# Performance work log

Hardware: AMD Instinct MI355X
Metric: run time of the kernel (lower is better)

Reference implementation:

```python
import jax, jax.numpy as jnp
import numpy as np

B, S, DM, H, D = 2, 2048, 1024, 16, 64

def setup_inputs() -> dict:
    key = jax.random.key(0)
    ks = jax.random.split(key, 9)
    def g(k, shape, scale=0.02):
        return jax.random.normal(k, shape, dtype=jnp.float32) * scale
    return {
        "x":  jax.random.normal(ks[0], (B, S, DM), dtype=jnp.float32),
        "Wq": g(ks[1], (DM, H * D)), "bq": g(ks[2], (H * D,)),
        "Wk": g(ks[3], (DM, H * D)), "bk": g(ks[4], (H * D,)),
        "Wv": g(ks[5], (DM, H * D)), "bv": g(ks[6], (H * D,)),
        "Wo": g(ks[7], (H * D, DM)), "bo": g(ks[8], (DM,)),
    }

def reference(x, Wq, bq, Wk, bk, Wv, bv, Wo, bo):
    b, s, _ = x.shape
    # projections -> (B, H, S, D)
    q = (x @ Wq + bq).reshape(b, s, H, D).transpose(0, 2, 1, 3)
    k = (x @ Wk + bk).reshape(b, s, H, D).transpose(0, 2, 1, 3)
    v = (x @ Wv + bv).reshape(b, s, H, D).transpose(0, 2, 1, 3)
    # naive attention: full (B,H,S,S) scores, causal mask, softmax
    scores = jnp.einsum("bhqd,bhkd->bhqk", q, k) / jnp.sqrt(jnp.float32(D))
    causal = jnp.tril(jnp.ones((s, s), dtype=bool))
    scores = jnp.where(causal[None, None], scores, jnp.float32(-jnp.inf))
    weights = jax.nn.softmax(scores, axis=-1)
    out = jnp.einsum("bhqk,bhkd->bhqd", weights, v)  # (B,H,S,D)
    out = out.transpose(0, 2, 1, 3).reshape(b, s, H * D)
    return out @ Wo + bo  # dropout_p = 0 -> identity
```

## Files before the change

### kernel.cpp

```cpp
#include <hip/hip_runtime.h>
#include <hip/hip_bf16.h>

typedef __hip_bfloat16 bf16;
typedef __attribute__((ext_vector_type(8))) short bf16x8;
typedef __attribute__((ext_vector_type(4))) float f32x4;
typedef __attribute__((ext_vector_type(4))) unsigned int u32x4;

#define MFMA_BF16(a, b, c) __builtin_amdgcn_mfma_f32_16x16x32_bf16((a), (b), (c), 0, 0, 0)

static constexpr int B_  = 2;
static constexpr int S_  = 2048;
static constexpr int DM_ = 1024;
static constexpr int H_  = 16;
static constexpr int D_  = 64;
static constexpr int M_  = B_ * S_;

__device__ __forceinline__ void load16(const void* g, void* l) {
  __builtin_amdgcn_global_load_lds(
      (const __attribute__((address_space(1))) void*)g,
      (__attribute__((address_space(3))) void*)l, 16, 0, 0);
}

__device__ __forceinline__ unsigned int pack_bf16(float lo, float hi) {
  const unsigned int ul = __builtin_bit_cast(unsigned short, __float2bfloat16(lo));
  const unsigned int uh = __builtin_bit_cast(unsigned short, __float2bfloat16(hi));
  return (uh << 16) | ul;
}


__global__ void cvt_f32_bf16_kernel(const float* __restrict__ in,
                                    bf16* __restrict__ out, int n4) {
  int i = blockIdx.x * blockDim.x + threadIdx.x;
  if (i >= n4) return;
  float4 v = ((const float4*)in)[i];
  ushort4 u;
  u.x = __builtin_bit_cast(unsigned short, __float2bfloat16(v.x));
  u.y = __builtin_bit_cast(unsigned short, __float2bfloat16(v.y));
  u.z = __builtin_bit_cast(unsigned short, __float2bfloat16(v.z));
  u.w = __builtin_bit_cast(unsigned short, __float2bfloat16(v.w));
  ((ushort4*)out)[i] = u;
}

__global__ void transpose_cvt_kernel(const float* __restrict__ w0,
                                     const float* __restrict__ w1,
                                     const float* __restrict__ w2,
                                     const float* __restrict__ w3,
                                     bf16* __restrict__ o0, bf16* __restrict__ o1,
                                     bf16* __restrict__ o2, bf16* __restrict__ o3) {
  __shared__ float t[32][33];
  const float* in = blockIdx.z == 0 ? w0 : blockIdx.z == 1 ? w1 : blockIdx.z == 2 ? w2 : w3;
  bf16* out = blockIdx.z == 0 ? o0 : blockIdx.z == 1 ? o1 : blockIdx.z == 2 ? o2 : o3;
  int tx = threadIdx.x & 31;
  int ty = threadIdx.x >> 5;
  int r0 = blockIdx.y * 32;
  int c0 = blockIdx.x * 32;
#pragma unroll
  for (int yy = 0; yy < 32; yy += 8)
    t[ty + yy][tx] = in[(size_t)(r0 + ty + yy) * DM_ + c0 + tx];
  __syncthreads();
#pragma unroll
  for (int yy = 0; yy < 32; yy += 8)
    out[(size_t)(c0 + ty + yy) * DM_ + r0 + tx] = __float2bfloat16(t[tx][ty + yy]);
}

template <int MODE>
__global__ __launch_bounds__(256) void gemm_bt_kernel(
    const bf16* __restrict__ A, const bf16* __restrict__ Bt,
    const float* __restrict__ bias, const float* __restrict__ bias2,
    const float* __restrict__ bias3, void* __restrict__ out, int K) {
  __shared__ bf16 As[128 * 32];
  __shared__ bf16 Bs[128 * 32];
  const int tid = threadIdx.x;
  const int wid = tid >> 6, lane = tid & 63;
  const int g = lane >> 4, c = lane & 15;
  const int wr = wid >> 1, wc = wid & 1;
  const int bm = blockIdx.x, bn = blockIdx.y;

  f32x4 acc[4][4] = {};

  const char* Ag = (const char*)(A + (size_t)bm * 128 * K);
  const char* Bg = (const char*)(Bt + (size_t)bn * 128 * K);
  const int f0 = tid * 16, f1 = f0 + 4096;
  const int r0 = f0 >> 6, cb0 = f0 & 63;
  const int r1 = f1 >> 6;
  const size_t rowbytes = (size_t)K * 2;

  for (int kt = 0; kt < K / 32; ++kt) {
    const size_t koff = (size_t)kt * 64;
    load16(Ag + (size_t)r0 * rowbytes + koff + cb0, (char*)As + f0);
    load16(Ag + (size_t)r1 * rowbytes + koff + cb0, (char*)As + f1);
    load16(Bg + (size_t)r0 * rowbytes + koff + cb0, (char*)Bs + f0);
    load16(Bg + (size_t)r1 * rowbytes + koff + cb0, (char*)Bs + f1);
    __syncthreads();
    bf16x8 af[4], bfr[4];
#pragma unroll
    for (int mi = 0; mi < 4; ++mi)
      af[mi] = *(const bf16x8*)&As[(wr * 64 + mi * 16 + c) * 32 + g * 8];
#pragma unroll
    for (int ni = 0; ni < 4; ++ni)
      bfr[ni] = *(const bf16x8*)&Bs[(wc * 64 + ni * 16 + c) * 32 + g * 8];
#pragma unroll
    for (int mi = 0; mi < 4; ++mi)
#pragma unroll
      for (int ni = 0; ni < 4; ++ni)
        acc[mi][ni] = MFMA_BF16(af[mi], bfr[ni], acc[mi][ni]);
    __syncthreads();
  }

#pragma unroll
  for (int ni = 0; ni < 4; ++ni) {
    const int n_g = bn * 128 + wc * 64 + ni * 16 + c;
    float bv;
    if constexpr (MODE == 3) {
      const int proj = n_g >> 10, ncol = n_g & 1023;
      bv = proj == 0 ? bias[ncol] : proj == 1 ? bias2[ncol] : bias3[ncol];
    } else {
      bv = bias[n_g];
    }
#pragma unroll
    for (int mi = 0; mi < 4; ++mi) {
#pragma unroll
      for (int r = 0; r < 4; ++r) {
        const int m_g = bm * 128 + wr * 64 + mi * 16 + g * 4 + r;
        const float val = acc[mi][ni][r] + bv;
        if constexpr (MODE == 2) {
          ((float*)out)[(size_t)m_g * DM_ + n_g] = val;
        } else {
          const int proj = n_g >> 10, ncol = n_g & 1023;
          const int b = m_g >> 11, s = m_g & (S_ - 1);
          const int h = ncol >> 6, d = ncol & (D_ - 1);
          size_t idx = (size_t)proj * 4194304;
          if (proj < 2)
            idx += (((size_t)(b * H_ + h)) * S_ + s) * D_ + d;
          else
            idx += (((size_t)(b * H_ + h)) * D_ + d) * S_ + s;
          ((bf16*)out)[idx] = __float2bfloat16(val);
        }
      }
    }
  }
}

__global__ __launch_bounds__(256, 4) void flash_attn_kernel(
    const bf16* __restrict__ Q, const bf16* __restrict__ Kg,
    const bf16* __restrict__ Vt, bf16* __restrict__ Aout) {
  __shared__ bf16 Ks[2][64 * 64];
  __shared__ bf16 Vs[2][64 * 64];
  const int tid = threadIdx.x;
  const int w = tid >> 6, lane = tid & 63;
  const int g = lane >> 4, c = lane & 15;

  const int bid = blockIdx.x;
  const int xcd = bid & 7, loc = bid >> 3;
  const int bh = xcd * 4 + (loc & 3);
  const int j = 31 - (loc >> 2);
  const int t = j * 4 + w;
  const int b = bh >> 4, h = bh & (H_ - 1);

  const float ALPHA2 = 0.125f * 1.44269504f;
  const float THR2 = 11.5f;
  const float NEG_INF = -__builtin_inff();

  const char* Kbase = (const char*)(Kg + (size_t)bh * S_ * D_);
  const char* Vbase = (const char*)(Vt + (size_t)bh * D_ * S_);
  const int s0 = tid, s1 = tid + 256;
  const int sr0 = s0 >> 3, sq0 = ((s0 & 7) ^ (sr0 & 7)) << 4;
  const int sr1 = s1 >> 3, sq1 = ((s1 & 7) ^ (sr1 & 7)) << 4;

  const bf16* Qp = Q + ((size_t)bh * S_ + t * 16 + c) * D_;
  bf16x8 qf[2];
  qf[0] = *(const bf16x8*)&Qp[g * 8];
  qf[1] = *(const bf16x8*)&Qp[32 + g * 8];

  f32x4 o[4] = {};
  float m = -1000.0f;
  float lsum = 0.0f;

  const int rowlim = w * 16 + c;
  const int src0 = ((g & 1) * 2) * 16 + c;
  const int src1 = src0 + 16;
  const bool ghi = (g >= 2);
  const int cs = c & 7;
  int roff[2][4];
#pragma unroll
  for (int kk = 0; kk < 2; ++kk)
#pragma unroll
    for (int n = 0; n < 4; ++n)
      roff[kk][n] = n * 2048 + c * 128 + (((kk * 4 + g) ^ cs) << 4);

  {
    const char* Krow = Kbase;
    const char* Vcol = Vbase;
    load16(Krow + sr0 * 128 + sq0, (char*)Ks[0] + s0 * 16);
    load16(Krow + sr1 * 128 + sq1, (char*)Ks[0] + s1 * 16);
    load16(Vcol + sr0 * 4096 + sq0, (char*)Vs[0] + s0 * 16);
    load16(Vcol + sr1 * 4096 + sq1, (char*)Vs[0] + s1 * 16);
  }
  __syncthreads();

  int cur = 0;
#pragma unroll 1
  for (int kv = 0; kv <= j; ++kv) {
    if (kv < j) {
      const char* Krow = Kbase + (size_t)(kv + 1) * 8192;
      const char* Vcol = Vbase + (size_t)(kv + 1) * 128;
      const int nb = cur ^ 1;
      load16(Krow + sr0 * 128 + sq0, (char*)Ks[nb] + s0 * 16);
      load16(Krow + sr1 * 128 + sq1, (char*)Ks[nb] + s1 * 16);
      load16(Vcol + sr0 * 4096 + sq0, (char*)Vs[nb] + s0 * 16);
      load16(Vcol + sr1 * 4096 + sq1, (char*)Vs[nb] + s1 * 16);
    }

    const char* Kt = (const char*)Ks[cur];
    const char* Vtile = (const char*)Vs[cur];
    bf16x8 kf[2][4];
#pragma unroll
    for (int kk = 0; kk < 2; ++kk)
#pragma unroll
      for (int n = 0; n < 4; ++n)
        kf[kk][n] = *(const bf16x8*)(Kt + roff[kk][n]);

    f32x4 st[4] = {};
#pragma unroll
    for (int n = 0; n < 4; ++n) {
      st[n] = MFMA_BF16(kf[0][n], qf[0], st[n]);
      st[n] = MFMA_BF16(kf[1][n], qf[1], st[n]);
    }

    bf16x8 vf[2][4];
#pragma unroll
    for (int kk = 0; kk < 2; ++kk)
#pragma unroll
      for (int n = 0; n < 4; ++n)
        vf[kk][n] = *(const bf16x8*)(Vtile + roff[kk][n]);

    float a[4][4];
#pragma unroll
    for (int n = 0; n < 4; ++n)
#pragma unroll
      for (int r = 0; r < 4; ++r)
        a[n][r] = fmaf(st[n][r], ALPHA2, -m);
    if (kv == j) {
#pragma unroll
      for (int n = 0; n < 4; ++n)
#pragma unroll
        for (int r = 0; r < 4; ++r)
          if (n * 16 + g * 4 + r > rowlim) a[n][r] = NEG_INF;
    }

    float dm;
    {
      float t0 = fmaxf(fmaxf(a[0][0], a[0][1]), fmaxf(a[0][2], a[0][3]));
      float t1 = fmaxf(fmaxf(a[1][0], a[1][1]), fmaxf(a[1][2], a[1][3]));
      float t2 = fmaxf(fmaxf(a[2][0], a[2][1]), fmaxf(a[2][2], a[2][3]));
      float t3 = fmaxf(fmaxf(a[3][0], a[3][1]), fmaxf(a[3][2], a[3][3]));
      dm = fmaxf(fmaxf(t0, t1), fmaxf(t2, t3));
    }
    dm = fmaxf(dm, __shfl_xor(dm, 16, 64));
    dm = fmaxf(dm, __shfl_xor(dm, 32, 64));

    if (__any(dm > THR2)) {
      const float sh = fmaxf(dm, 0.0f);
      const float sc = __builtin_amdgcn_exp2f(-sh);
      m += sh;
      lsum *= sc;
#pragma unroll
      for (int n = 0; n < 4; ++n)
#pragma unroll
        for (int r = 0; r < 4; ++r) o[n][r] *= sc;
#pragma unroll
      for (int n = 0; n < 4; ++n)
#pragma unroll
        for (int r = 0; r < 4; ++r) a[n][r] -= sh;
    }

    float p[4][4];
#pragma unroll
    for (int n = 0; n < 4; ++n)
#pragma unroll
      for (int r = 0; r < 4; ++r) p[n][r] = __builtin_amdgcn_exp2f(a[n][r]);
    {
      float q0 = (p[0][0] + p[0][1]) + (p[0][2] + p[0][3]);
      float q1 = (p[1][0] + p[1][1]) + (p[1][2] + p[1][3]);
      float q2 = (p[2][0] + p[2][1]) + (p[2][2] + p[2][3]);
      float q3 = (p[3][0] + p[3][1]) + (p[3][2] + p[3][3]);
      lsum += (q0 + q1) + (q2 + q3);
    }

    unsigned int dw[4][2];
#pragma unroll
    for (int n = 0; n < 4; ++n) {
      dw[n][0] = pack_bf16(p[n][0], p[n][1]);
      dw[n][1] = pack_bf16(p[n][2], p[n][3]);
    }

#pragma unroll
    for (int kk = 0; kk < 2; ++kk) {
      unsigned int bb[4];
      {
        unsigned int lo = __shfl(dw[kk * 2][0], src0, 64);
        unsigned int hi = __shfl(dw[kk * 2 + 1][0], src0, 64);
        bb[0] = ghi ? hi : lo;
      }
      {
        unsigned int lo = __shfl(dw[kk * 2][1], src0, 64);
        unsigned int hi = __shfl(dw[kk * 2 + 1][1], src0, 64);
        bb[1] = ghi ? hi : lo;
      }
      {
        unsigned int lo = __shfl(dw[kk * 2][0], src1, 64);
        unsigned int hi = __shfl(dw[kk * 2 + 1][0], src1, 64);
        bb[2] = ghi ? hi : lo;
      }
      {
        unsigned int lo = __shfl(dw[kk * 2][1], src1, 64);
        unsigned int hi = __shfl(dw[kk * 2 + 1][1], src1, 64);
        bb[3] = ghi ? hi : lo;
      }
      u32x4 bbv = {bb[0], bb[1], bb[2], bb[3]};
      bf16x8 pb = __builtin_bit_cast(bf16x8, bbv);
#pragma unroll
      for (int n = 0; n < 4; ++n) o[n] = MFMA_BF16(vf[kk][n], pb, o[n]);
    }

    __syncthreads();
    cur ^= 1;
  }

  lsum += __shfl_xor(lsum, 16, 64);
  lsum += __shfl_xor(lsum, 32, 64);
  const float inv = 1.0f / lsum;

  bf16* Arow = Aout + ((size_t)b * S_ + t * 16 + c) * (H_ * D_) + h * D_;
#pragma unroll
  for (int n = 0; n < 4; ++n) {
    ushort4 u;
    u.x = __builtin_bit_cast(unsigned short, __float2bfloat16(o[n][0] * inv));
    u.y = __builtin_bit_cast(unsigned short, __float2bfloat16(o[n][1] * inv));
    u.z = __builtin_bit_cast(unsigned short, __float2bfloat16(o[n][2] * inv));
    u.w = __builtin_bit_cast(unsigned short, __float2bfloat16(o[n][3] * inv));
    *(ushort4*)&Arow[n * 16 + g * 4] = u;
  }
}


extern "C" void kernel_launch(void* const* d_in, const int* in_sizes, int n_in,
                              void* d_out, int out_size, void* d_ws, size_t ws_size,
                              hipStream_t stream) {
  (void)in_sizes; (void)n_in; (void)out_size; (void)ws_size;
  const float* x  = (const float*)d_in[0];
  const float* Wq = (const float*)d_in[1];
  const float* bq = (const float*)d_in[2];
  const float* Wk = (const float*)d_in[3];
  const float* bk = (const float*)d_in[4];
  const float* Wv = (const float*)d_in[5];
  const float* bv = (const float*)d_in[6];
  const float* Wo = (const float*)d_in[7];
  const float* bo = (const float*)d_in[8];
  float* out = (float*)d_out;

  char* ws = (char*)d_ws;
  bf16* xb  = (bf16*)(ws);
  bf16* Wqt = (bf16*)(ws + (8u << 20));
  bf16* Wkt = (bf16*)(ws + (10u << 20));
  bf16* Wvt = (bf16*)(ws + (12u << 20));
  bf16* Wot = (bf16*)(ws + (14u << 20));
  bf16* Qb  = (bf16*)(ws + (16u << 20));
  bf16* Kb  = (bf16*)(ws + (24u << 20));
  bf16* Vtb = (bf16*)(ws + (32u << 20));
  bf16* Ab  = xb;

  cvt_f32_bf16_kernel<<<4096, 256, 0, stream>>>(x, xb, (M_ * DM_) / 4);
  transpose_cvt_kernel<<<dim3(32, 32, 4), 256, 0, stream>>>(
      Wq, Wk, Wv, Wo, Wqt, Wkt, Wvt, Wot);

  gemm_bt_kernel<3><<<dim3(32, 24), 256, 0, stream>>>(
      xb, Wqt, bq, bk, bv, (void*)Qb, DM_);

  flash_attn_kernel<<<dim3(1024), 256, 0, stream>>>(Qb, Kb, Vtb, Ab);

  gemm_bt_kernel<2><<<dim3(32, 8), 256, 0, stream>>>(
      Ab, Wot, bo, nullptr, nullptr, (void*)out, DM_);
}
```

Before: 127.8 us.

## Pair causal query tiles per block and triple-buffer KV with setprio

Each attention block now handles two query tiles, j and 31-j, so causal work is balanced across blocks, and the grid is halved to 512. KV staging moves from a double to a triple buffer with a prefetch distance of two, explicit vmcnt waits and a single barrier per iteration. s_setprio is raised around the MFMA groups. The aim is to remove tail imbalance and hide load latency, at the cost of more LDS per block (48KB), which may limit occupancy, and half as many blocks.

```diff
diff --git a/kernel.cpp b/kernel.cpp
--- a/kernel.cpp
+++ b/kernel.cpp
@@ -144,8 +144,7 @@
 __global__ __launch_bounds__(256, 4) void flash_attn_kernel(
     const bf16* __restrict__ Q, const bf16* __restrict__ Kg,
     const bf16* __restrict__ Vt, bf16* __restrict__ Aout) {
-  __shared__ bf16 Ks[2][64 * 64];
-  __shared__ bf16 Vs[2][64 * 64];
+  __shared__ bf16 KVs[3][2][64 * 64];
   const int tid = threadIdx.x;
   const int w = tid >> 6, lane = tid & 63;
   const int g = lane >> 4, c = lane & 15;
@@ -153,8 +152,7 @@
   const int bid = blockIdx.x;
   const int xcd = bid & 7, loc = bid >> 3;
   const int bh = xcd * 4 + (loc & 3);
-  const int j = 31 - (loc >> 2);
-  const int t = j * 4 + w;
+  const int pp = loc >> 2;
   const int b = bh >> 4, h = bh & (H_ - 1);
 
   const float ALPHA2 = 0.125f * 1.44269504f;
@@ -167,14 +165,14 @@
   const int sr0 = s0 >> 3, sq0 = ((s0 & 7) ^ (sr0 & 7)) << 4;
   const int sr1 = s1 >> 3, sq1 = ((s1 & 7) ^ (sr1 & 7)) << 4;
 
-  const bf16* Qp = Q + ((size_t)bh * S_ + t * 16 + c) * D_;
-  bf16x8 qf[2];
-  qf[0] = *(const bf16x8*)&Qp[g * 8];
-  qf[1] = *(const bf16x8*)&Qp[32 + g * 8];
-
-  f32x4 o[4] = {};
-  float m = -1000.0f;
-  float lsum = 0.0f;
+  auto stageKV = [&](int kv, int bufi) {
+    const char* Krow = Kbase + (size_t)kv * 8192;
+    const char* Vcol = Vbase + (size_t)kv * 128;
+    load16(Krow + sr0 * 128 + sq0, (char*)KVs[bufi][0] + s0 * 16);
+    load16(Krow + sr1 * 128 + sq1, (char*)KVs[bufi][0] + s1 * 16);
+    load16(Vcol + sr0 * 4096 + sq0, (char*)KVs[bufi][1] + s0 * 16);
+    load16(Vcol + sr1 * 4096 + sq1, (char*)KVs[bufi][1] + s1 * 16);
+  };
 
   const int rowlim = w * 16 + c;
   const int src0 = ((g & 1) * 2) * 16 + c;
@@ -188,158 +186,169 @@
     for (int n = 0; n < 4; ++n)
       roff[kk][n] = n * 2048 + c * 128 + (((kk * 4 + g) ^ cs) << 4);
 
-  {
-    const char* Krow = Kbase;
-    const char* Vcol = Vbase;
-    load16(Krow + sr0 * 128 + sq0, (char*)Ks[0] + s0 * 16);
-    load16(Krow + sr1 * 128 + sq1, (char*)Ks[0] + s1 * 16);
-    load16(Vcol + sr0 * 4096 + sq0, (char*)Vs[0] + s0 * 16);
-    load16(Vcol + sr1 * 4096 + sq1, (char*)Vs[0] + s1 * 16);
-  }
-  __syncthreads();
-
-  int cur = 0;
 #pragma unroll 1
-  for (int kv = 0; kv <= j; ++kv) {
-    if (kv < j) {
-      const char* Krow = Kbase + (size_t)(kv + 1) * 8192;
-      const char* Vcol = Vbase + (size_t)(kv + 1) * 128;
-      const int nb = cur ^ 1;
-      load16(Krow + sr0 * 128 + sq0, (char*)Ks[nb] + s0 * 16);
-      load16(Krow + sr1 * 128 + sq1, (char*)Ks[nb] + s1 * 16);
-      load16(Vcol + sr0 * 4096 + sq0, (char*)Vs[nb] + s0 * 16);
-      load16(Vcol + sr1 * 4096 + sq1, (char*)Vs[nb] + s1 * 16);
+  for (int pass = 0; pass < 2; ++pass) {
+    const int j = pass == 0 ? pp : 31 - pp;
+    const int t16 = j * 4 + w;
+
+    const bf16* Qp = Q + ((size_t)bh * S_ + t16 * 16 + c) * D_;
+    bf16x8 qf[2];
+    qf[0] = *(const bf16x8*)&Qp[g * 8];
+    qf[1] = *(const bf16x8*)&Qp[32 + g * 8];
+
+    f32x4 o[4] = {};
+    float m = -1000.0f;
+    float lsum = 0.0f;
+
+    stageKV(0, 0);
+    if (j >= 1) stageKV(1, 1);
+
+    int cb = 0;
+#pragma unroll 1
+    for (int kv = 0; kv <= j; ++kv) {
+      if (kv < j) asm volatile("s_waitcnt vmcnt(4)" ::: "memory");
+      else        asm volatile("s_waitcnt vmcnt(0)" ::: "memory");
+      __builtin_amdgcn_s_barrier();
+      if (kv + 2 <= j) {
+        int sb = cb + 2; if (sb >= 3) sb -= 3;
+        stageKV(kv + 2, sb);
+      }
+
+      const char* Kt = (const char*)KVs[cb][0];
+      const char* Vtile = (const char*)KVs[cb][1];
+      bf16x8 kf[2][4];
+#pragma unroll
+      for (int kk = 0; kk < 2; ++kk)
+#pragma unroll
+        for (int n = 0; n < 4; ++n)
+          kf[kk][n] = *(const bf16x8*)(Kt + roff[kk][n]);
+
+      f32x4 st[4] = {};
+      __builtin_amdgcn_s_setprio(1);
+#pragma unroll
+      for (int n = 0; n < 4; ++n) {
+        st[n] = MFMA_BF16(kf[0][n], qf[0], st[n]);
+        st[n] = MFMA_BF16(kf[1][n], qf[1], st[n]);
+      }
+      __builtin_amdgcn_s_setprio(0);
+
+      bf16x8 vf[2][4];
+#pragma unroll
+      for (int kk = 0; kk < 2; ++kk)
+#pragma unroll
+        for (int n = 0; n < 4; ++n)
+          vf[kk][n] = *(const bf16x8*)(Vtile + roff[kk][n]);
+
+      float a[4][4];
+#pragma unroll
+      for (int n = 0; n < 4; ++n)
+#pragma unroll
+        for (int r = 0; r < 4; ++r)
+          a[n][r] = fmaf(st[n][r], ALPHA2, -m);
+      if (kv == j) {
+#pragma unroll
+        for (int n = 0; n < 4; ++n)
+#pragma unroll
+          for (int r = 0; r < 4; ++r)
+            if (n * 16 + g * 4 + r > rowlim) a[n][r] = NEG_INF;
+      }
+
+      float dm;
+      {
+        float t0 = fmaxf(fmaxf(a[0][0], a[0][1]), fmaxf(a[0][2], a[0][3]));
+        float t1 = fmaxf(fmaxf(a[1][0], a[1][1]), fmaxf(a[1][2], a[1][3]));
+        float t2 = fmaxf(fmaxf(a[2][0], a[2][1]), fmaxf(a[2][2], a[2][3]));
+        float t3 = fmaxf(fmaxf(a[3][0], a[3][1]), fmaxf(a[3][2], a[3][3]));
+        dm = fmaxf(fmaxf(t0, t1), fmaxf(t2, t3));
+      }
+      dm = fmaxf(dm, __shfl_xor(dm, 16, 64));
+      dm = fmaxf(dm, __shfl_xor(dm, 32, 64));
+
+      if (__any(dm > THR2)) {
+        const float sh = fmaxf(dm, 0.0f);
+        const float sc = __builtin_amdgcn_exp2f(-sh);
+        m += sh;
+        lsum *= sc;
+#pragma unroll
+        for (int n = 0; n < 4; ++n)
+#pragma unroll
+          for (int r = 0; r < 4; ++r) o[n][r] *= sc;
+#pragma unroll
+        for (int n = 0; n < 4; ++n)
+#pragma unroll
+          for (int r = 0; r < 4; ++r) a[n][r] -= sh;
+      }
+
+      float p[4][4];
+#pragma unroll
+      for (int n = 0; n < 4; ++n)
+#pragma unroll
+        for (int r = 0; r < 4; ++r) p[n][r] = __builtin_amdgcn_exp2f(a[n][r]);
+      {
+        float q0 = (p[0][0] + p[0][1]) + (p[0][2] + p[0][3]);
+        float q1 = (p[1][0] + p[1][1]) + (p[1][2] + p[1][3]);
+        float q2 = (p[2][0] + p[2][1]) + (p[2][2] + p[2][3]);
+        float q3 = (p[3][0] + p[3][1]) + (p[3][2] + p[3][3]);
+        lsum += (q0 + q1) + (q2 + q3);
+      }
+
+      unsigned int dw[4][2];
+#pragma unroll
+      for (int n = 0; n < 4; ++n) {
+        dw[n][0] = pack_bf16(p[n][0], p[n][1]);
+        dw[n][1] = pack_bf16(p[n][2], p[n][3]);
+      }
+
+#pragma unroll
+      for (int kk = 0; kk < 2; ++kk) {
+        unsigned int bb[4];
+        {
+          unsigned int lo = __shfl(dw[kk * 2][0], src0, 64);
+          unsigned int hi = __shfl(dw[kk * 2 + 1][0], src0, 64);
+          bb[0] = ghi ? hi : lo;
+        }
+        {
+          unsigned int lo = __shfl(dw[kk * 2][1], src0, 64);
+          unsigned int hi = __shfl(dw[kk * 2 + 1][1], src0, 64);
+          bb[1] = ghi ? hi : lo;
+        }
+        {
+          unsigned int lo = __shfl(dw[kk * 2][0], src1, 64);
+          unsigned int hi = __shfl(dw[kk * 2 + 1][0], src1, 64);
+          bb[2] = ghi ? hi : lo;
+        }
+        {
+          unsigned int lo = __shfl(dw[kk * 2][1], src1, 64);
+          unsigned int hi = __shfl(dw[kk * 2 + 1][1], src1, 64);
+          bb[3] = ghi ? hi : lo;
+        }
+        u32x4 bbv = {bb[0], bb[1], bb[2], bb[3]};
+        bf16x8 pb = __builtin_bit_cast(bf16x8, bbv);
+        __builtin_amdgcn_s_setprio(1);
+#pragma unroll
+        for (int n = 0; n < 4; ++n) o[n] = MFMA_BF16(vf[kk][n], pb, o[n]);
+        __builtin_amdgcn_s_setprio(0);
+      }
+
+      cb = (cb == 2) ? 0 : cb + 1;
     }
 
-    const char* Kt = (const char*)Ks[cur];
-    const char* Vtile = (const char*)Vs[cur];
-    bf16x8 kf[2][4];
-#pragma unroll
-    for (int kk = 0; kk < 2; ++kk)
-#pragma unroll
-      for (int n = 0; n < 4; ++n)
-        kf[kk][n] = *(const bf16x8*)(Kt + roff[kk][n]);
-
-    f32x4 st[4] = {};
+    lsum += __shfl_xor(lsum, 16, 64);
+    lsum += __shfl_xor(lsum, 32, 64);
+    const float inv = 1.0f / lsum;
+
+    bf16* Arow = Aout + ((size_t)b * S_ + t16 * 16 + c) * (H_ * D_) + h * D_;
 #pragma unroll
     for (int n = 0; n < 4; ++n) {
-      st[n] = MFMA_BF16(kf[0][n], qf[0], st[n]);
-      st[n] = MFMA_BF16(kf[1][n], qf[1], st[n]);
+      ushort4 u;
+      u.x = __builtin_bit_cast(unsigned short, __float2bfloat16(o[n][0] * inv));
+      u.y = __builtin_bit_cast(unsigned short, __float2bfloat16(o[n][1] * inv));
+      u.z = __builtin_bit_cast(unsigned short, __float2bfloat16(o[n][2] * inv));
+      u.w = __builtin_bit_cast(unsigned short, __float2bfloat16(o[n][3] * inv));
+      *(ushort4*)&Arow[n * 16 + g * 4] = u;
     }
 
-    bf16x8 vf[2][4];
-#pragma unroll
-    for (int kk = 0; kk < 2; ++kk)
-#pragma unroll
-      for (int n = 0; n < 4; ++n)
-        vf[kk][n] = *(const bf16x8*)(Vtile + roff[kk][n]);
-
-    float a[4][4];
-#pragma unroll
-    for (int n = 0; n < 4; ++n)
-#pragma unroll
-      for (int r = 0; r < 4; ++r)
-        a[n][r] = fmaf(st[n][r], ALPHA2, -m);
-    if (kv == j) {
-#pragma unroll
-      for (int n = 0; n < 4; ++n)
-#pragma unroll
-        for (int r = 0; r < 4; ++r)
-          if (n * 16 + g * 4 + r > rowlim) a[n][r] = NEG_INF;
-    }
-
-    float dm;
-    {
-      float t0 = fmaxf(fmaxf(a[0][0], a[0][1]), fmaxf(a[0][2], a[0][3]));
-      float t1 = fmaxf(fmaxf(a[1][0], a[1][1]), fmaxf(a[1][2], a[1][3]));
-      float t2 = fmaxf(fmaxf(a[2][0], a[2][1]), fmaxf(a[2][2], a[2][3]));
-      float t3 = fmaxf(fmaxf(a[3][0], a[3][1]), fmaxf(a[3][2], a[3][3]));
-      dm = fmaxf(fmaxf(t0, t1), fmaxf(t2, t3));
-    }
-    dm = fmaxf(dm, __shfl_xor(dm, 16, 64));
-    dm = fmaxf(dm, __shfl_xor(dm, 32, 64));
-
-    if (__any(dm > THR2)) {
-      const float sh = fmaxf(dm, 0.0f);
-      const float sc = __builtin_amdgcn_exp2f(-sh);
-      m += sh;
-      lsum *= sc;
-#pragma unroll
-      for (int n = 0; n < 4; ++n)
-#pragma unroll
-        for (int r = 0; r < 4; ++r) o[n][r] *= sc;
-#pragma unroll
-      for (int n = 0; n < 4; ++n)
-#pragma unroll
-        for (int r = 0; r < 4; ++r) a[n][r] -= sh;
-    }
-
-    float p[4][4];
-#pragma unroll
-    for (int n = 0; n < 4; ++n)
-#pragma unroll
-      for (int r = 0; r < 4; ++r) p[n][r] = __builtin_amdgcn_exp2f(a[n][r]);
-    {
-      float q0 = (p[0][0] + p[0][1]) + (p[0][2] + p[0][3]);
-      float q1 = (p[1][0] + p[1][1]) + (p[1][2] + p[1][3]);
-      float q2 = (p[2][0] + p[2][1]) + (p[2][2] + p[2][3]);
-      float q3 = (p[3][0] + p[3][1]) + (p[3][2] + p[3][3]);
-      lsum += (q0 + q1) + (q2 + q3);
-    }
-
-    unsigned int dw[4][2];
-#pragma unroll
-    for (int n = 0; n < 4; ++n) {
-      dw[n][0] = pack_bf16(p[n][0], p[n][1]);
-      dw[n][1] = pack_bf16(p[n][2], p[n][3]);
-    }
-
-#pragma unroll
-    for (int kk = 0; kk < 2; ++kk) {
-      unsigned int bb[4];
-      {
-        unsigned int lo = __shfl(dw[kk * 2][0], src0, 64);
-        unsigned int hi = __shfl(dw[kk * 2 + 1][0], src0, 64);
-        bb[0] = ghi ? hi : lo;
-      }
-      {
-        unsigned int lo = __shfl(dw[kk * 2][1], src0, 64);
-        unsigned int hi = __shfl(dw[kk * 2 + 1][1], src0, 64);
-        bb[1] = ghi ? hi : lo;
-      }
-      {
-        unsigned int lo = __shfl(dw[kk * 2][0], src1, 64);
-        unsigned int hi = __shfl(dw[kk * 2 + 1][0], src1, 64);
-        bb[2] = ghi ? hi : lo;
-      }
-      {
-        unsigned int lo = __shfl(dw[kk * 2][1], src1, 64);
-        unsigned int hi = __shfl(dw[kk * 2 + 1][1], src1, 64);
-        bb[3] = ghi ? hi : lo;
-      }
-      u32x4 bbv = {bb[0], bb[1], bb[2], bb[3]};
-      bf16x8 pb = __builtin_bit_cast(bf16x8, bbv);
-#pragma unroll
-      for (int n = 0; n < 4; ++n) o[n] = MFMA_BF16(vf[kk][n], pb, o[n]);
-    }
-
     __syncthreads();
-    cur ^= 1;
-  }
-
-  lsum += __shfl_xor(lsum, 16, 64);
-  lsum += __shfl_xor(lsum, 32, 64);
-  const float inv = 1.0f / lsum;
-
-  bf16* Arow = Aout + ((size_t)b * S_ + t * 16 + c) * (H_ * D_) + h * D_;
-#pragma unroll
-  for (int n = 0; n < 4; ++n) {
-    ushort4 u;
-    u.x = __builtin_bit_cast(unsigned short, __float2bfloat16(o[n][0] * inv));
-    u.y = __builtin_bit_cast(unsigned short, __float2bfloat16(o[n][1] * inv));
-    u.z = __builtin_bit_cast(unsigned short, __float2bfloat16(o[n][2] * inv));
-    u.w = __builtin_bit_cast(unsigned short, __float2bfloat16(o[n][3] * inv));
-    *(ushort4*)&Arow[n * 16 + g * 4] = u;
   }
 }
 
@@ -377,7 +386,7 @@
   gemm_bt_kernel<3><<<dim3(32, 24), 256, 0, stream>>>(
       xb, Wqt, bq, bk, bv, (void*)Qb, DM_);
 
-  flash_attn_kernel<<<dim3(1024), 256, 0, stream>>>(Qb, Kb, Vtb, Ab);
+  flash_attn_kernel<<<dim3(512), 256, 0, stream>>>(Qb, Kb, Vtb, Ab);
 
   gemm_bt_kernel<2><<<dim3(32, 8), 256, 0, stream>>>(
       Ab, Wot, bo, nullptr, nullptr, (void*)out, DM_);
```

Result: slower. 132.6 us (+3.8%).

## Double-buffer GEMM LDS tiles and raise wave priority around MFMA blocks

Applied to the files above, without the earlier changes.

The projection GEMM kernel moves from a single LDS buffer with two syncthreads per k-step to a double-buffered scheme. The next tile's global-to-LDS loads are issued before computing on the current tile, with manual vmcnt waits and raw barriers. s_setprio bumps are also wrapped around MFMA sequences in both the GEMM and the attention kernel so other waves' memory instructions can interleave. This doubles GEMM LDS use, which may reduce occupancy, and relies on hand-placed waitcnt correctness.

```diff
diff --git a/kernel.cpp b/kernel.cpp
--- a/kernel.cpp
+++ b/kernel.cpp
@@ -68,8 +68,8 @@
     const bf16* __restrict__ A, const bf16* __restrict__ Bt,
     const float* __restrict__ bias, const float* __restrict__ bias2,
     const float* __restrict__ bias3, void* __restrict__ out, int K) {
-  __shared__ bf16 As[128 * 32];
-  __shared__ bf16 Bs[128 * 32];
+  __shared__ bf16 As[2][128 * 32];
+  __shared__ bf16 Bs[2][128 * 32];
   const int tid = threadIdx.x;
   const int wid = tid >> 6, lane = tid & 63;
   const int g = lane >> 4, c = lane & 15;
@@ -85,26 +85,44 @@
   const int r1 = f1 >> 6;
   const size_t rowbytes = (size_t)K * 2;
 
-  for (int kt = 0; kt < K / 32; ++kt) {
+  auto stage = [&](int kt, int bufi) {
     const size_t koff = (size_t)kt * 64;
-    load16(Ag + (size_t)r0 * rowbytes + koff + cb0, (char*)As + f0);
-    load16(Ag + (size_t)r1 * rowbytes + koff + cb0, (char*)As + f1);
-    load16(Bg + (size_t)r0 * rowbytes + koff + cb0, (char*)Bs + f0);
-    load16(Bg + (size_t)r1 * rowbytes + koff + cb0, (char*)Bs + f1);
-    __syncthreads();
+    load16(Ag + (size_t)r0 * rowbytes + koff + cb0, (char*)As[bufi] + f0);
+    load16(Ag + (size_t)r1 * rowbytes + koff + cb0, (char*)As[bufi] + f1);
+    load16(Bg + (size_t)r0 * rowbytes + koff + cb0, (char*)Bs[bufi] + f0);
+    load16(Bg + (size_t)r1 * rowbytes + koff + cb0, (char*)Bs[bufi] + f1);
+  };
+
+  const int NT = K / 32;
+  stage(0, 0);
+  int cur = 0;
+#pragma unroll 1
+  for (int kt = 0; kt < NT; ++kt) {
+    if (kt + 1 < NT) {
+      stage(kt + 1, cur ^ 1);
+      asm volatile("s_waitcnt vmcnt(4)" ::: "memory");
+    } else {
+      asm volatile("s_waitcnt vmcnt(0)" ::: "memory");
+    }
+    __builtin_amdgcn_s_barrier();
+
     bf16x8 af[4], bfr[4];
 #pragma unroll
     for (int mi = 0; mi < 4; ++mi)
-      af[mi] = *(const bf16x8*)&As[(wr * 64 + mi * 16 + c) * 32 + g * 8];
+      af[mi] = *(const bf16x8*)&As[cur][(wr * 64 + mi * 16 + c) * 32 + g * 8];
 #pragma unroll
     for (int ni = 0; ni < 4; ++ni)
-      bfr[ni] = *(const bf16x8*)&Bs[(wc * 64 + ni * 16 + c) * 32 + g * 8];
+      bfr[ni] = *(const bf16x8*)&Bs[cur][(wc * 64 + ni * 16 + c) * 32 + g * 8];
+    __builtin_amdgcn_s_setprio(1);
 #pragma unroll
     for (int mi = 0; mi < 4; ++mi)
 #pragma unroll
       for (int ni = 0; ni < 4; ++ni)
         acc[mi][ni] = MFMA_BF16(af[mi], bfr[ni], acc[mi][ni]);
-    __syncthreads();
+    __builtin_amdgcn_s_setprio(0);
+
+    if (kt + 1 < NT) __builtin_amdgcn_s_barrier();
+    cur ^= 1;
   }
 
 #pragma unroll
@@ -189,12 +207,10 @@
       roff[kk][n] = n * 2048 + c * 128 + (((kk * 4 + g) ^ cs) << 4);
 
   {
-    const char* Krow = Kbase;
-    const char* Vcol = Vbase;
-    load16(Krow + sr0 * 128 + sq0, (char*)Ks[0] + s0 * 16);
-    load16(Krow + sr1 * 128 + sq1, (char*)Ks[0] + s1 * 16);
-    load16(Vcol + sr0 * 4096 + sq0, (char*)Vs[0] + s0 * 16);
-    load16(Vcol + sr1 * 4096 + sq1, (char*)Vs[0] + s1 * 16);
+    load16(Kbase + sr0 * 128 + sq0, (char*)Ks[0] + s0 * 16);
+    load16(Kbase + sr1 * 128 + sq1, (char*)Ks[0] + s1 * 16);
+    load16(Vbase + sr0 * 4096 + sq0, (char*)Vs[0] + s0 * 16);
+    load16(Vbase + sr1 * 4096 + sq1, (char*)Vs[0] + s1 * 16);
   }
   __syncthreads();
 
@@ -221,11 +237,13 @@
         kf[kk][n] = *(const bf16x8*)(Kt + roff[kk][n]);
 
     f32x4 st[4] = {};
+    __builtin_amdgcn_s_setprio(1);
 #pragma unroll
     for (int n = 0; n < 4; ++n) {
       st[n] = MFMA_BF16(kf[0][n], qf[0], st[n]);
       st[n] = MFMA_BF16(kf[1][n], qf[1], st[n]);
     }
+    __builtin_amdgcn_s_setprio(0);
 
     bf16x8 vf[2][4];
 #pragma unroll
@@ -319,8 +337,10 @@
       }
       u32x4 bbv = {bb[0], bb[1], bb[2], bb[3]};
       bf16x8 pb = __builtin_bit_cast(bf16x8, bbv);
+      __builtin_amdgcn_s_setprio(1);
 #pragma unroll
       for (int n = 0; n < 4; ++n) o[n] = MFMA_BF16(vf[kk][n], pb, o[n]);
+      __builtin_amdgcn_s_setprio(0);
     }
 
     __syncthreads();
```

New measurement: 121.6 us. 1.05x faster.
